# Optimization experiments

Hardware: AMD Instinct MI355X
Metric: run time of the kernel (lower is better)

Reference implementation:

```python
import jax, jax.numpy as jnp
import numpy as np

# Model dims (match init_kwargs)
E, D, H, K = 8, 512, 1024, 2   # num_experts, input/output dim, hidden dim, top_k
B, S = 4, 2048                 # batch, seq_len


def setup_inputs() -> dict:
    key = jax.random.key(0)
    ks = jax.random.split(key, 5)
    sd = lambda fan: np.float32(1.0 / np.sqrt(fan))
    return {
        "x": jax.random.normal(ks[0], (B, S, D), jnp.float32),
        "gate_w": jax.random.normal(ks[1], (D, E), jnp.float32) * sd(D),
        "gate_b": jnp.zeros((E,), jnp.float32),
        "w1": jax.random.normal(ks[2], (E, D, H), jnp.float32) * sd(D),
        "b1": jnp.zeros((E, H), jnp.float32),
        "w2": jax.random.normal(ks[3], (E, H, D), jnp.float32) * sd(H),
        "b2": jnp.zeros((E, D), jnp.float32),
    }


def reference(x, gate_w, gate_b, w1, b1, w2, b2):
    # x: [B, S, D]
    Bb, Ss, Dd = x.shape
    xf = x.reshape(-1, Dd)                              # [N, D], N = B*S

    # Router: softmax over experts, top-k, renormalize selected weights
    logits = xf @ gate_w + gate_b                        # [N, E]
    probs = jax.nn.softmax(logits, axis=-1)              # [N, E]
    top_w, top_i = jax.lax.top_k(probs, K)               # [N, K]
    top_w = top_w / top_w.sum(axis=-1, keepdims=True)

    # Per-token combine weight for each expert (0 if not routed).
    onehot = jax.nn.one_hot(top_i, E, dtype=probs.dtype)  # [N, K, E]
    combine = jnp.einsum("nke,nk->ne", onehot, top_w)     # [N, E]

    # Expert MLPs. Dropout is inactive at inference (identity).
    # h: [E, N, H]; GELU exact (torch nn.GELU default uses erf)
    h = jax.nn.gelu(jnp.einsum("nd,edh->enh", xf, w1) + b1[:, None, :],
                    approximate=False)
    y = jnp.einsum("enh,ehd->end", h, w2) + b2[:, None, :]  # [E, N, D]

    # Weighted combine: tokens not routed to expert e have combine[:, e] == 0.
    out = jnp.einsum("end,ne->nd", y, combine).reshape(Bb, Ss, Dd)
    return out, probs.reshape(Bb, Ss, E)
```

## Files before the change

kernel.cpp:

```cpp
#include <hip/hip_runtime.h>
#include <stdint.h>

#define N_TOK 8192
#define DIM   512
#define HID   1024
#define NE    8
#define NSLOT 16384
#define MAXSLOT 17408

typedef __attribute__((ext_vector_type(8))) short short8;
typedef __attribute__((ext_vector_type(4))) float f32x4;

#define W1T_OFF  0ull
#define W2T_OFF  8388608ull
#define H_OFF    16777216ull
#define Y_OFF    52428800ull
#define XBF_OFF  52428800ull
#define TOPI_OFF 70254592ull
#define TOPW_OFF 70320128ull
#define SLOT_OFF 70385664ull
#define ROWS_OFF 70451200ull
#define RW_OFF   70520832ull
#define CNT_OFF  70590464ull

__device__ __forceinline__ unsigned int f2bfu(float f) {
  union { float f; unsigned int i; } v; v.f = f;
  unsigned int u = v.i;
  return (u + 0x7FFFu + ((u >> 16) & 1u)) >> 16;
}
__device__ __forceinline__ float bf2f(unsigned int u) {
  union { unsigned int i; float f; } v; v.i = (u & 0xFFFFu) << 16; return v.f;
}
__device__ __forceinline__ float gelu_f(float x) {
  float x2 = x * x;
  float u = x * (1.59576912f + 0.07135481f * x2);
  float ez = __expf(-u);
  return x * __builtin_amdgcn_rcpf(1.0f + ez);
}
__device__ __forceinline__ void async16(void* lds, const void* g) {
  __builtin_amdgcn_global_load_lds(
      (const __attribute__((address_space(1))) unsigned int*)g,
      (__attribute__((address_space(3))) unsigned int*)lds, 16, 0, 0);
}

__global__ __launch_bounds__(256) void k_transpose(
    const float* __restrict__ w1, const float* __restrict__ w2,
    unsigned short* __restrict__ w1t, unsigned short* __restrict__ w2t) {
  __shared__ unsigned short tile[64][68];
  int b = blockIdx.x, tid = threadIdx.x;
  const float* src; unsigned short* dst; int R, C;
  if (b < 1024) { int e = b >> 7; int t = b & 127;
    src = w1 + (size_t)e * 524288; dst = w1t + (size_t)e * 524288; R = 512; C = 1024;
    int tr = t >> 4, tc = t & 15;
    src += (size_t)tr * 64 * C + tc * 64; dst += (size_t)tc * 64 * R + tr * 64;
  } else { b -= 1024; int e = b >> 7; int t = b & 127;
    src = w2 + (size_t)e * 524288; dst = w2t + (size_t)e * 524288; R = 1024; C = 512;
    int tr = t >> 3, tc = t & 7;
    src += (size_t)tr * 64 * C + tc * 64; dst += (size_t)tc * 64 * R + tr * 64;
  }
#pragma unroll
  for (int i = 0; i < 4; ++i) {
    int l = i * 256 + tid;
    int r = l >> 4, c4 = (l & 15) << 2;
    float4 v = *(const float4*)(src + (size_t)r * C + c4);
    tile[r][c4 + 0] = (unsigned short)f2bfu(v.x);
    tile[r][c4 + 1] = (unsigned short)f2bfu(v.y);
    tile[r][c4 + 2] = (unsigned short)f2bfu(v.z);
    tile[r][c4 + 3] = (unsigned short)f2bfu(v.w);
  }
  __syncthreads();
#pragma unroll
  for (int i = 0; i < 4; ++i) {
    int l = i * 256 + tid;
    int rr = l >> 4, c4 = (l & 15) << 2;
    ushort4 v;
    v.x = tile[c4 + 0][rr]; v.y = tile[c4 + 1][rr]; v.z = tile[c4 + 2][rr]; v.w = tile[c4 + 3][rr];
    *(ushort4*)(dst + (size_t)rr * R + c4) = v;
  }
}

__global__ __launch_bounds__(256) void k_router(
    const float* __restrict__ x, const float* __restrict__ gw,
    const float* __restrict__ gb, float* __restrict__ probs_out,
    int2* __restrict__ topi, float2* __restrict__ topw,
    unsigned short* __restrict__ xbf) {
  int wave = threadIdx.x >> 6, lane = threadIdx.x & 63;
  int n = blockIdx.x * 4 + wave;
  const float4* xr = (const float4*)(x + (size_t)n * DIM);
  float4 x0 = xr[lane * 2], x1 = xr[lane * 2 + 1];
  float xf[8] = {x0.x, x0.y, x0.z, x0.w, x1.x, x1.y, x1.z, x1.w};
  uint4 pa;
  pa.x = f2bfu(xf[0]) | (f2bfu(xf[1]) << 16);
  pa.y = f2bfu(xf[2]) | (f2bfu(xf[3]) << 16);
  pa.z = f2bfu(xf[4]) | (f2bfu(xf[5]) << 16);
  pa.w = f2bfu(xf[6]) | (f2bfu(xf[7]) << 16);
  *(uint4*)(xbf + (size_t)n * DIM + lane * 8) = pa;
  float acc[8] = {0.f,0.f,0.f,0.f,0.f,0.f,0.f,0.f};
  const float4* gwr = (const float4*)gw;
#pragma unroll
  for (int j = 0; j < 8; ++j) {
    int d = lane * 8 + j;
    float4 g0 = gwr[d * 2], g1 = gwr[d * 2 + 1];
    acc[0] += xf[j] * g0.x; acc[1] += xf[j] * g0.y; acc[2] += xf[j] * g0.z; acc[3] += xf[j] * g0.w;
    acc[4] += xf[j] * g1.x; acc[5] += xf[j] * g1.y; acc[6] += xf[j] * g1.z; acc[7] += xf[j] * g1.w;
  }
#pragma unroll
  for (int o = 1; o < 64; o <<= 1)
#pragma unroll
    for (int e = 0; e < 8; ++e) acc[e] += __shfl_xor(acc[e], o, 64);
  float p[8], mx = -1e30f, s = 0.f;
#pragma unroll
  for (int e = 0; e < 8; ++e) { p[e] = acc[e] + gb[e]; mx = fmaxf(mx, p[e]); }
#pragma unroll
  for (int e = 0; e < 8; ++e) { p[e] = __expf(p[e] - mx); s += p[e]; }
  float inv = 1.f / s;
#pragma unroll
  for (int e = 0; e < 8; ++e) p[e] *= inv;
  if (lane < 8) probs_out[(size_t)n * NE + lane] = p[lane];
  if (lane == 0) {
    int i0 = 0; float v0 = p[0];
#pragma unroll
    for (int e = 1; e < 8; ++e) if (p[e] > v0) { v0 = p[e]; i0 = e; }
    int i1 = -1; float v1 = -1.f;
#pragma unroll
    for (int e = 0; e < 8; ++e) if (e != i0 && p[e] > v1) { v1 = p[e]; i1 = e; }
    float sw = 1.f / (v0 + v1);
    topi[n] = make_int2(i0, i1);
    topw[n] = make_float2(v0 * sw, v1 * sw);
  }
}

__global__ __launch_bounds__(1024) void k_count(
    const int2* __restrict__ topi, int* __restrict__ meta, int* __restrict__ chunk_base,
    int* __restrict__ rows, float* __restrict__ rw) {
  __shared__ int ch[32][8];
  __shared__ int tot[8], poff_s[9], tiles_s[8];
  int t = threadIdx.x;
  int g = t >> 5;
  if (t < 256) ((int*)ch)[t] = 0;
  __syncthreads();
  int c[8] = {0,0,0,0,0,0,0,0};
  int base_tok = t * 8;
#pragma unroll
  for (int i = 0; i < 8; ++i) {
    int2 e = topi[base_tok + i];
#pragma unroll
    for (int k = 0; k < 8; ++k) c[k] += (e.x == k) + (e.y == k);
  }
#pragma unroll
  for (int k = 0; k < 8; ++k) if (c[k]) atomicAdd(&ch[g][k], c[k]);
  __syncthreads();
  if (t < 8) {
    int a = 0;
#pragma unroll
    for (int b = 0; b < 32; ++b) { int v = ch[b][t]; ch[b][t] = a; a += v; }
    tot[t] = a; meta[t] = a;
  }
  __syncthreads();
  if (t == 0) {
    int a = 0, ts = 0;
#pragma unroll
    for (int e = 0; e < 8; ++e) {
      int tiles = (tot[e] + 127) >> 7;
      poff_s[e] = a; tiles_s[e] = tiles;
      meta[16 + e] = a; meta[32 + e] = ts;
      a += tiles << 7; ts += tiles;
    }
    poff_s[8] = a; meta[24] = a; meta[40] = ts;
  }
  __syncthreads();
  if (t < 256) {
    int b = t >> 3, e = t & 7;
    chunk_base[t] = poff_s[e] + ch[b][e];
  }
#pragma unroll
  for (int e = 0; e < 8; ++e) {
    int padn = (tiles_s[e] << 7) - tot[e];
    if (t < padn) {
      int s = poff_s[e] + tot[e] + t;
      rows[s] = 0; rw[s] = 0.f;
    }
  }
}

__global__ __launch_bounds__(256) void k_assign(
    const int2* __restrict__ topi, const float2* __restrict__ topw,
    const int* __restrict__ chunk_base,
    int* __restrict__ rows, float* __restrict__ rw, int* __restrict__ slot_of) {
  __shared__ int lcnt[8];
  __shared__ int lbase[8];
  int t = threadIdx.x, b = blockIdx.x;
  if (t < 8) { lcnt[t] = 0; lbase[t] = chunk_base[b * 8 + t]; }
  __syncthreads();
  int n = b * 256 + t;
  int2 ei = topi[n]; float2 wv = topw[n];
  int r0 = atomicAdd(&lcnt[ei.x], 1);
  int r1 = atomicAdd(&lcnt[ei.y], 1);
  int s0 = lbase[ei.x] + r0;
  int s1 = lbase[ei.y] + r1;
  rows[s0] = n; rw[s0] = wv.x; slot_of[2 * n] = s0;
  rows[s1] = n; rw[s1] = wv.y; slot_of[2 * n + 1] = s1;
}

__global__ __launch_bounds__(256) void k_gemm1(
    const unsigned short* __restrict__ xbf, const unsigned short* __restrict__ w1t,
    const float* __restrict__ b1, const int* __restrict__ meta,
    const int* __restrict__ rows, unsigned short* __restrict__ h) {
  int t = blockIdx.x;
  if (t >= meta[40]) return;
  int e = 0;
#pragma unroll
  for (int i = 1; i < 8; ++i) if (t >= meta[32 + i]) e = i;
  int mt = t - meta[32 + e];
  int row0 = meta[16 + e] + (mt << 7);
  int nt = blockIdx.y;
  __shared__ __align__(16) unsigned short As[128 * 64];
  __shared__ __align__(16) unsigned short Bs[128 * 64];
  __shared__ int rows_l[128];
  int tid = threadIdx.x;
  if (tid < 128) rows_l[tid] = rows[row0 + tid];
  __syncthreads();
  int wave = tid >> 6, lane = tid & 63;
  int wr = wave & 1, wc = wave >> 1;
  f32x4 acc[4][4] = {};
  const unsigned short* bBase = w1t + (size_t)e * HID * DIM + (size_t)(nt * 128) * DIM;

  const unsigned short* ga[4]; const unsigned short* gb[4];
#pragma unroll
  for (int j = 0; j < 4; ++j) {
    int s = j * 256 + tid;
    int r = s >> 3;
    int cg = ((s & 7) ^ (r & 7)) << 3;
    ga[j] = xbf + (size_t)rows_l[r] * DIM + cg;
    gb[j] = bBase + (size_t)r * DIM + cg;
  }

  for (int k0 = 0; k0 < DIM; k0 += 64) {
#pragma unroll
    for (int j = 0; j < 4; ++j) {
      async16(&As[(j * 256 + wave * 64) * 8], ga[j] + k0);
      async16(&Bs[(j * 256 + wave * 64) * 8], gb[j] + k0);
    }
    __syncthreads();
#pragma unroll
    for (int kk = 0; kk < 2; ++kk) {
      int ca = kk * 4 + (lane >> 4);
      short8 tf[4], wf[4];
#pragma unroll
      for (int am = 0; am < 4; ++am) {
        int ra = wr * 64 + am * 16 + (lane & 15);
        tf[am] = *(const short8*)&As[(ra * 8 + (ca ^ (ra & 7))) * 8];
      }
#pragma unroll
      for (int an = 0; an < 4; ++an) {
        int rb = wc * 64 + an * 16 + (lane & 15);
        wf[an] = *(const short8*)&Bs[(rb * 8 + (ca ^ (rb & 7))) * 8];
      }
#pragma unroll
      for (int an = 0; an < 4; ++an)
#pragma unroll
        for (int am = 0; am < 4; ++am)
          acc[an][am] = __builtin_amdgcn_mfma_f32_16x16x32_bf16(wf[an], tf[am], acc[an][am], 0, 0, 0);
    }
    __syncthreads();
  }
  int ml = lane & 15, q = lane >> 4;
#pragma unroll
  for (int am = 0; am < 4; ++am) {
    int slot_r = row0 + wr * 64 + am * 16 + ml;
    unsigned short* hrow = h + (size_t)slot_r * HID;
#pragma unroll
    for (int an = 0; an < 4; ++an) {
      int colb = nt * 128 + wc * 64 + an * 16 + q * 4;
      float4 bias = *(const float4*)&b1[e * HID + colb];
      f32x4 v = acc[an][am];
      float g0 = gelu_f(v[0] + bias.x);
      float g1 = gelu_f(v[1] + bias.y);
      float g2 = gelu_f(v[2] + bias.z);
      float g3 = gelu_f(v[3] + bias.w);
      uint2 pk;
      pk.x = f2bfu(g0) | (f2bfu(g1) << 16);
      pk.y = f2bfu(g2) | (f2bfu(g3) << 16);
      *(uint2*)(hrow + colb) = pk;
    }
  }
}

__global__ __launch_bounds__(256) void k_gemm2(
    const unsigned short* __restrict__ h, const unsigned short* __restrict__ w2t,
    const float* __restrict__ b2, const int* __restrict__ meta,
    const float* __restrict__ rw, unsigned short* __restrict__ y) {
  int t = blockIdx.x;
  if (t >= meta[40]) return;
  int e = 0;
#pragma unroll
  for (int i = 1; i < 8; ++i) if (t >= meta[32 + i]) e = i;
  int mt = t - meta[32 + e];
  int row0 = meta[16 + e] + (mt << 7);
  int nt = blockIdx.y;
  __shared__ __align__(16) unsigned short As[128 * 64];
  __shared__ __align__(16) unsigned short Bs[128 * 64];
  int tid = threadIdx.x;
  int wave = tid >> 6, lane = tid & 63;
  int wr = wave & 1, wc = wave >> 1;
  f32x4 acc[4][4] = {};
  const unsigned short* aBase = h + (size_t)row0 * HID;
  const unsigned short* bBase = w2t + (size_t)e * DIM * HID + (size_t)(nt * 128) * HID;

  const unsigned short* ga[4]; const unsigned short* gb[4];
#pragma unroll
  for (int j = 0; j < 4; ++j) {
    int s = j * 256 + tid;
    int r = s >> 3;
    int cg = ((s & 7) ^ (r & 7)) << 3;
    ga[j] = aBase + (size_t)r * HID + cg;
    gb[j] = bBase + (size_t)r * HID + cg;
  }

  for (int k0 = 0; k0 < HID; k0 += 64) {
#pragma unroll
    for (int j = 0; j < 4; ++j) {
      async16(&As[(j * 256 + wave * 64) * 8], ga[j] + k0);
      async16(&Bs[(j * 256 + wave * 64) * 8], gb[j] + k0);
    }
    __syncthreads();
#pragma unroll
    for (int kk = 0; kk < 2; ++kk) {
      int ca = kk * 4 + (lane >> 4);
      short8 tf[4], wf[4];
#pragma unroll
      for (int am = 0; am < 4; ++am) {
        int ra = wr * 64 + am * 16 + (lane & 15);
        tf[am] = *(const short8*)&As[(ra * 8 + (ca ^ (ra & 7))) * 8];
      }
#pragma unroll
      for (int an = 0; an < 4; ++an) {
        int rb = wc * 64 + an * 16 + (lane & 15);
        wf[an] = *(const short8*)&Bs[(rb * 8 + (ca ^ (rb & 7))) * 8];
      }
#pragma unroll
      for (int an = 0; an < 4; ++an)
#pragma unroll
        for (int am = 0; am < 4; ++am)
          acc[an][am] = __builtin_amdgcn_mfma_f32_16x16x32_bf16(wf[an], tf[am], acc[an][am], 0, 0, 0);
    }
    __syncthreads();
  }
  int ml = lane & 15, q = lane >> 4;
#pragma unroll
  for (int am = 0; am < 4; ++am) {
    int slot_r = row0 + wr * 64 + am * 16 + ml;
    float w = rw[slot_r];
    unsigned short* yrow = y + (size_t)slot_r * DIM;
#pragma unroll
    for (int an = 0; an < 4; ++an) {
      int colb = nt * 128 + wc * 64 + an * 16 + q * 4;
      float4 bias = *(const float4*)&b2[e * DIM + colb];
      f32x4 v = acc[an][am];
      uint2 pk;
      pk.x = f2bfu((v[0] + bias.x) * w) | (f2bfu((v[1] + bias.y) * w) << 16);
      pk.y = f2bfu((v[2] + bias.z) * w) | (f2bfu((v[3] + bias.w) * w) << 16);
      *(uint2*)(yrow + colb) = pk;
    }
  }
}

__global__ __launch_bounds__(256) void k_combine(
    const unsigned short* __restrict__ y, const int* __restrict__ slot_of,
    float* __restrict__ out) {
  int t = blockIdx.x * 256 + threadIdx.x;
  int n = t >> 6, c = (t & 63) << 3;
  int s0 = slot_of[2 * n], s1 = slot_of[2 * n + 1];
  uint4 u0 = *(const uint4*)(y + (size_t)s0 * DIM + c);
  uint4 u1 = *(const uint4*)(y + (size_t)s1 * DIM + c);
  float4 o0, o1;
  o0.x = bf2f(u0.x) + bf2f(u1.x); o0.y = bf2f(u0.x >> 16) + bf2f(u1.x >> 16);
  o0.z = bf2f(u0.y) + bf2f(u1.y); o0.w = bf2f(u0.y >> 16) + bf2f(u1.y >> 16);
  o1.x = bf2f(u0.z) + bf2f(u1.z); o1.y = bf2f(u0.z >> 16) + bf2f(u1.z >> 16);
  o1.z = bf2f(u0.w) + bf2f(u1.w); o1.w = bf2f(u0.w >> 16) + bf2f(u1.w >> 16);
  *(float4*)(out + (size_t)n * DIM + c) = o0;
  *(float4*)(out + (size_t)n * DIM + c + 4) = o1;
}

extern "C" void kernel_launch(void* const* d_in, const int* in_sizes, int n_in,
                              void* d_out, int out_size, void* d_ws, size_t ws_size,
                              hipStream_t stream) {
  const float* x  = (const float*)d_in[0];
  const float* gw = (const float*)d_in[1];
  const float* gb = (const float*)d_in[2];
  const float* w1 = (const float*)d_in[3];
  const float* b1 = (const float*)d_in[4];
  const float* w2 = (const float*)d_in[5];
  const float* b2 = (const float*)d_in[6];
  float* out = (float*)d_out;
  char* ws = (char*)d_ws;

  unsigned short* w1t = (unsigned short*)(ws + W1T_OFF);
  unsigned short* w2t = (unsigned short*)(ws + W2T_OFF);
  unsigned short* h   = (unsigned short*)(ws + H_OFF);
  unsigned short* y   = (unsigned short*)(ws + Y_OFF);
  unsigned short* xbf = (unsigned short*)(ws + XBF_OFF);
  int2*   topi    = (int2*)(ws + TOPI_OFF);
  float2* topw    = (float2*)(ws + TOPW_OFF);
  int*    slot_of = (int*)(ws + SLOT_OFF);
  int*    rows    = (int*)(ws + ROWS_OFF);
  float*  rw      = (float*)(ws + RW_OFF);
  int*    meta    = (int*)(ws + CNT_OFF);
  int*    chunk_base = meta + 64;
  float*  probs   = out + (size_t)N_TOK * DIM;

  k_transpose<<<dim3(2048), dim3(256), 0, stream>>>(w1, w2, w1t, w2t);
  k_router   <<<dim3(2048), dim3(256), 0, stream>>>(x, gw, gb, probs, topi, topw, xbf);
  k_count    <<<dim3(1),    dim3(1024), 0, stream>>>(topi, meta, chunk_base, rows, rw);
  k_assign   <<<dim3(32),   dim3(256), 0, stream>>>(topi, topw, chunk_base, rows, rw, slot_of);
  k_gemm1    <<<dim3(136, 8), dim3(256), 0, stream>>>(xbf, w1t, b1, meta, rows, h);
  k_gemm2    <<<dim3(136, 4), dim3(256), 0, stream>>>(h, w2t, b2, meta, rw, y);
  k_combine  <<<dim3(2048), dim3(256), 0, stream>>>(y, slot_of, out);
}
```

Before: 214.3 us.

## Double-buffer LDS tiles in expert GEMMs and make the N-tile the fast grid axis

Both expert GEMM kernels now keep two LDS buffers for the A and B tiles. The global-to-LDS async copy for the next K-step is issued before the MFMA work on the current step, so memory latency can overlap compute instead of each iteration loading, syncing and then computing. The grid axes are also swapped so adjacent blocks share the same row tile across N-tiles, which should improve L2 reuse of the gathered activations. The row-index staging through shared memory is dropped in favour of direct global reads. The cost is twice the LDS per block (64KB), which can lower occupancy.

```diff
diff --git a/kernel.cpp b/kernel.cpp
--- a/kernel.cpp
+++ b/kernel.cpp
@@ -206,20 +206,17 @@
     const unsigned short* __restrict__ xbf, const unsigned short* __restrict__ w1t,
     const float* __restrict__ b1, const int* __restrict__ meta,
     const int* __restrict__ rows, unsigned short* __restrict__ h) {
-  int t = blockIdx.x;
+  int t = blockIdx.y;
   if (t >= meta[40]) return;
   int e = 0;
 #pragma unroll
   for (int i = 1; i < 8; ++i) if (t >= meta[32 + i]) e = i;
   int mt = t - meta[32 + e];
   int row0 = meta[16 + e] + (mt << 7);
-  int nt = blockIdx.y;
-  __shared__ __align__(16) unsigned short As[128 * 64];
-  __shared__ __align__(16) unsigned short Bs[128 * 64];
-  __shared__ int rows_l[128];
+  int nt = blockIdx.x;
+  __shared__ __align__(16) unsigned short As[2][8192];
+  __shared__ __align__(16) unsigned short Bs[2][8192];
   int tid = threadIdx.x;
-  if (tid < 128) rows_l[tid] = rows[row0 + tid];
-  __syncthreads();
   int wave = tid >> 6, lane = tid & 63;
   int wr = wave & 1, wc = wave >> 1;
   f32x4 acc[4][4] = {};
@@ -231,17 +228,27 @@
     int s = j * 256 + tid;
     int r = s >> 3;
     int cg = ((s & 7) ^ (r & 7)) << 3;
-    ga[j] = xbf + (size_t)rows_l[r] * DIM + cg;
+    ga[j] = xbf + (size_t)rows[row0 + r] * DIM + cg;
     gb[j] = bBase + (size_t)r * DIM + cg;
   }
+  int ldst = (wave * 64) * 8;
+
+#pragma unroll
+  for (int j = 0; j < 4; ++j) {
+    async16(&As[0][j * 2048 + ldst], ga[j]);
+    async16(&Bs[0][j * 2048 + ldst], gb[j]);
+  }
+  __syncthreads();
 
   for (int k0 = 0; k0 < DIM; k0 += 64) {
-#pragma unroll
-    for (int j = 0; j < 4; ++j) {
-      async16(&As[(j * 256 + wave * 64) * 8], ga[j] + k0);
-      async16(&Bs[(j * 256 + wave * 64) * 8], gb[j] + k0);
-    }
-    __syncthreads();
+    int cur = (k0 >> 6) & 1, nxt = cur ^ 1;
+    if (k0 + 64 < DIM) {
+#pragma unroll
+      for (int j = 0; j < 4; ++j) {
+        async16(&As[nxt][j * 2048 + ldst], ga[j] + k0 + 64);
+        async16(&Bs[nxt][j * 2048 + ldst], gb[j] + k0 + 64);
+      }
+    }
 #pragma unroll
     for (int kk = 0; kk < 2; ++kk) {
       int ca = kk * 4 + (lane >> 4);
@@ -249,12 +256,12 @@
 #pragma unroll
       for (int am = 0; am < 4; ++am) {
         int ra = wr * 64 + am * 16 + (lane & 15);
-        tf[am] = *(const short8*)&As[(ra * 8 + (ca ^ (ra & 7))) * 8];
+        tf[am] = *(const short8*)&As[cur][(ra * 8 + (ca ^ (ra & 7))) * 8];
       }
 #pragma unroll
       for (int an = 0; an < 4; ++an) {
         int rb = wc * 64 + an * 16 + (lane & 15);
-        wf[an] = *(const short8*)&Bs[(rb * 8 + (ca ^ (rb & 7))) * 8];
+        wf[an] = *(const short8*)&Bs[cur][(rb * 8 + (ca ^ (rb & 7))) * 8];
       }
 #pragma unroll
       for (int an = 0; an < 4; ++an)
@@ -290,16 +297,16 @@
     const unsigned short* __restrict__ h, const unsigned short* __restrict__ w2t,
     const float* __restrict__ b2, const int* __restrict__ meta,
     const float* __restrict__ rw, unsigned short* __restrict__ y) {
-  int t = blockIdx.x;
+  int t = blockIdx.y;
   if (t >= meta[40]) return;
   int e = 0;
 #pragma unroll
   for (int i = 1; i < 8; ++i) if (t >= meta[32 + i]) e = i;
   int mt = t - meta[32 + e];
   int row0 = meta[16 + e] + (mt << 7);
-  int nt = blockIdx.y;
-  __shared__ __align__(16) unsigned short As[128 * 64];
-  __shared__ __align__(16) unsigned short Bs[128 * 64];
+  int nt = blockIdx.x;
+  __shared__ __align__(16) unsigned short As[2][8192];
+  __shared__ __align__(16) unsigned short Bs[2][8192];
   int tid = threadIdx.x;
   int wave = tid >> 6, lane = tid & 63;
   int wr = wave & 1, wc = wave >> 1;
@@ -316,14 +323,24 @@
     ga[j] = aBase + (size_t)r * HID + cg;
     gb[j] = bBase + (size_t)r * HID + cg;
   }
+  int ldst = (wave * 64) * 8;
+
+#pragma unroll
+  for (int j = 0; j < 4; ++j) {
+    async16(&As[0][j * 2048 + ldst], ga[j]);
+    async16(&Bs[0][j * 2048 + ldst], gb[j]);
+  }
+  __syncthreads();
 
   for (int k0 = 0; k0 < HID; k0 += 64) {
-#pragma unroll
-    for (int j = 0; j < 4; ++j) {
-      async16(&As[(j * 256 + wave * 64) * 8], ga[j] + k0);
-      async16(&Bs[(j * 256 + wave * 64) * 8], gb[j] + k0);
-    }
-    __syncthreads();
+    int cur = (k0 >> 6) & 1, nxt = cur ^ 1;
+    if (k0 + 64 < HID) {
+#pragma unroll
+      for (int j = 0; j < 4; ++j) {
+        async16(&As[nxt][j * 2048 + ldst], ga[j] + k0 + 64);
+        async16(&Bs[nxt][j * 2048 + ldst], gb[j] + k0 + 64);
+      }
+    }
 #pragma unroll
     for (int kk = 0; kk < 2; ++kk) {
       int ca = kk * 4 + (lane >> 4);
@@ -331,12 +348,12 @@
 #pragma unroll
       for (int am = 0; am < 4; ++am) {
         int ra = wr * 64 + am * 16 + (lane & 15);
-        tf[am] = *(const short8*)&As[(ra * 8 + (ca ^ (ra & 7))) * 8];
+        tf[am] = *(const short8*)&As[cur][(ra * 8 + (ca ^ (ra & 7))) * 8];
       }
 #pragma unroll
       for (int an = 0; an < 4; ++an) {
         int rb = wc * 64 + an * 16 + (lane & 15);
-        wf[an] = *(const short8*)&Bs[(rb * 8 + (ca ^ (rb & 7))) * 8];
+        wf[an] = *(const short8*)&Bs[cur][(rb * 8 + (ca ^ (rb & 7))) * 8];
       }
 #pragma unroll
       for (int an = 0; an < 4; ++an)
@@ -413,7 +430,7 @@
   k_router   <<<dim3(2048), dim3(256), 0, stream>>>(x, gw, gb, probs, topi, topw, xbf);
   k_count    <<<dim3(1),    dim3(1024), 0, stream>>>(topi, meta, chunk_base, rows, rw);
   k_assign   <<<dim3(32),   dim3(256), 0, stream>>>(topi, topw, chunk_base, rows, rw, slot_of);
-  k_gemm1    <<<dim3(136, 8), dim3(256), 0, stream>>>(xbf, w1t, b1, meta, rows, h);
-  k_gemm2    <<<dim3(136, 4), dim3(256), 0, stream>>>(h, w2t, b2, meta, rw, y);
+  k_gemm1    <<<dim3(8, 136), dim3(256), 0, stream>>>(xbf, w1t, b1, meta, rows, h);
+  k_gemm2    <<<dim3(4, 136), dim3(256), 0, stream>>>(h, w2t, b2, meta, rw, y);
   k_combine  <<<dim3(2048), dim3(256), 0, stream>>>(y, slot_of, out);
 }
```

Result: no change. 214.2 us (-0.1%).
